# Optimization experiments

Measured on AMD Instinct MI355X. Metric: run time of the kernel, lower is better.

## Reference

```python
import jax, jax.numpy as jnp
import numpy as np

N = 100000   # nodes
E = 1600000  # edges
F = 128      # input features
H = 128      # hidden
O = 64       # output classes
BN_EPS = 1e-5


def gcn_conv(x, edge_index, W, b, n_nodes):
    """PyG-style GCNConv: h = D^-1/2 (A+I) D^-1/2 (x W) + b."""
    h = x @ W  # [N, out]
    row = jnp.concatenate([edge_index[0], jnp.arange(n_nodes)])  # add self loops
    col = jnp.concatenate([edge_index[1], jnp.arange(n_nodes)])
    deg = jax.ops.segment_sum(jnp.ones_like(row, dtype=h.dtype), row, num_segments=n_nodes)
    dinv = jnp.where(deg > 0, jax.lax.rsqrt(deg), 0.0)
    norm = dinv[row] * dinv[col]                 # [E+N]
    msg = h[col] * norm[:, None]                 # gather + scale
    out = jax.ops.segment_sum(msg, row, num_segments=n_nodes)  # scatter-add
    return out + b


def batch_norm(x, gamma, beta):
    mean = jnp.mean(x, axis=0)
    var = jnp.var(x, axis=0)
    return (x - mean) * jax.lax.rsqrt(var + BN_EPS) * gamma + beta


def setup_inputs() -> dict:
    key = jax.random.key(0)
    ks = jax.random.split(key, 10)
    x = jax.random.normal(ks[0], (N, F), dtype=jnp.float32)
    edge_index = jax.random.randint(ks[1], (2, E), 0, N, dtype=jnp.int64)
    W1 = jax.random.normal(ks[2], (F, H), dtype=jnp.float32) / np.sqrt(F)
    b1 = jnp.zeros((H,), dtype=jnp.float32)
    gamma1 = jnp.ones((H,), dtype=jnp.float32)
    beta1 = jnp.zeros((H,), dtype=jnp.float32)
    W2 = jax.random.normal(ks[3], (H, H), dtype=jnp.float32) / np.sqrt(H)
    b2 = jnp.zeros((H,), dtype=jnp.float32)
    W3 = jax.random.normal(ks[4], (H, O), dtype=jnp.float32) / np.sqrt(H)
    b3 = jnp.zeros((O,), dtype=jnp.float32)
    return {"x": x, "edge_index": edge_index, "W1": W1, "b1": b1,
            "gamma1": gamma1, "beta1": beta1, "W2": W2, "b2": b2,
            "W3": W3, "b3": b3}


def reference(x, edge_index, W1, b1, gamma1, beta1, W2, b2, W3, b3):
    h = gcn_conv(x, edge_index, W1, b1, N)
    h = jax.nn.relu(batch_norm(h, gamma1, beta1))
    h = gcn_conv(h, edge_index, W2, b2, N)
    h = jax.nn.relu(h)
    out = h @ W3 + b3  # final Linear classifier head [N, O]
    return out
```

## Files before the change

kernel.cpp:

```cpp
#include <hip/hip_runtime.h>

#define NN 100000
#define EE 1600000
#define HN 128
#define OO 64
#define SB 256
#define NBUCK 196
#define CH 4096
#define SLAB 16384

typedef __attribute__((ext_vector_type(8))) short bf16x8;
typedef __attribute__((ext_vector_type(4))) float f32x4;

__device__ __forceinline__ unsigned short f2bf(float f){
  unsigned u = __float_as_uint(f);
  return (unsigned short)((u + 0x7FFFu + ((u >> 16) & 1u)) >> 16);
}
__device__ __forceinline__ float bflo(unsigned u){ return __uint_as_float(u << 16); }
__device__ __forceinline__ float bfhi(unsigned u){ return __uint_as_float(u & 0xFFFF0000u); }

__global__ __launch_bounds__(256) void k_bucket(const int* __restrict__ rows, const int* __restrict__ cols,
                                                int* __restrict__ pcur, unsigned* __restrict__ ebuf,
                                                const float* __restrict__ W1, const float* __restrict__ W2,
                                                const float* __restrict__ W3,
                                                unsigned short* __restrict__ Wp1, unsigned short* __restrict__ Wp2,
                                                unsigned short* __restrict__ Wp3){
  __shared__ int bc[NBUCK];
  __shared__ int boff[NBUCK];
  __shared__ int ccur[NBUCK];
  __shared__ int gbase[NBUCK];
  __shared__ uint2 stage[CH];
  const int t = threadIdx.x;
  const int base = blockIdx.x * CH;
  const int nval = min(CH, EE - base);

  for (int i = t; i < NBUCK; i += 256) bc[i] = 0;
  __syncthreads();

  int er[16], ec[16];
  #pragma unroll
  for (int j = 0; j < 16; ++j){
    int i = j*256 + t;
    if (i < nval){
      er[j] = rows[base+i]; ec[j] = cols[base+i];
      atomicAdd(&bc[er[j] >> 9], 1);
    } else er[j] = -1;
  }
  __syncthreads();

  if (t < 64){
    int lane = t, run = 0;
    for (int c = 0; c < NBUCK; c += 64){
      int i = c + lane;
      int v = (i < NBUCK) ? bc[i] : 0;
      int s = v;
      #pragma unroll
      for (int d = 1; d < 64; d <<= 1){ int u = __shfl_up(s, d); if (lane >= d) s += u; }
      if (i < NBUCK) boff[i] = run + s - v;
      run += __shfl(s, 63);
    }
  }
  __syncthreads();
  if (t < NBUCK){
    gbase[t] = bc[t] ? (t*SLAB + atomicAdd(&pcur[t], bc[t])) : 0;
    ccur[t]  = boff[t];
  }
  __syncthreads();
  #pragma unroll
  for (int j = 0; j < 16; ++j){
    if (er[j] >= 0){
      int b = er[j] >> 9;
      int p = atomicAdd(&ccur[b], 1);
      stage[p] = make_uint2((unsigned)er[j], (unsigned)ec[j]);
    }
  }
  __syncthreads();
  for (int i = t; i < nval; i += 256){
    uint2 e = stage[i];
    int b = (int)(e.x >> 9);
    unsigned pk = ((e.x & 511u) << 17) | e.y;
    ebuf[gbase[b] + (i - boff[b])] = pk;
  }

  int b = blockIdx.x;
  if (b < 20){
    const float* W; unsigned short* Wp; int outc, i0;
    if (b < 8)      { W=W1; Wp=Wp1; outc=128; i0 = b*256; }
    else if (b < 16){ W=W2; Wp=Wp2; outc=128; i0 = (b-8)*256; }
    else            { W=W3; Wp=Wp3; outc=64;  i0 = (b-16)*256; }
    int i = i0 + t;
    if (i < 16*outc){
      int kb = i / outc, n = i - kb*outc;
      unsigned pk[4];
      #pragma unroll
      for (int jj = 0; jj < 4; ++jj){
        unsigned lo = f2bf(W[(size_t)(kb*8 + 2*jj)*outc + n]);
        unsigned hi = f2bf(W[(size_t)(kb*8 + 2*jj+1)*outc + n]);
        pk[jj] = lo | (hi << 16);
      }
      *reinterpret_cast<uint4*>(Wp + (size_t)i*8) = make_uint4(pk[0],pk[1],pk[2],pk[3]);
    }
  }
}

__global__ __launch_bounds__(256) void k_build(const unsigned* __restrict__ ebuf,
                                               const int* __restrict__ pcur,
                                               int* __restrict__ row_start, int* __restrict__ cnt,
                                               float* __restrict__ dinv, int* __restrict__ csr_col){
  __shared__ int hist[512];
  __shared__ int cur[512];
  __shared__ int sCbase;
  const int b = blockIdx.x;
  const int row0 = b << 9;
  const int nrow = min(512, NN - row0);
  const int ebase = b * SLAB;
  const int ne = pcur[b];
  const int t = threadIdx.x;

  if (t < 64){
    int acc = 0;
    for (int i = t; i < b; i += 64) acc += pcur[i];
    #pragma unroll
    for (int d = 32; d; d >>= 1) acc += __shfl_xor(acc, d);
    if (t == 0) sCbase = acc;
  }
  for (int i = t; i < nrow; i += 256) hist[i] = 0;
  __syncthreads();
  for (int i = t; i < ne; i += 256)
    atomicAdd(&hist[ebuf[ebase+i] >> 17], 1);
  __syncthreads();

  if (t < 64){
    int lane = t, run = 0;
    for (int c = 0; c < nrow; c += 64){
      int i = c + lane;
      int v = (i < nrow) ? hist[i] : 0;
      int s = v;
      #pragma unroll
      for (int d = 1; d < 64; d <<= 1){ int u = __shfl_up(s, d); if (lane >= d) s += u; }
      if (i < nrow) cur[i] = run + s - v;
      run += __shfl(s, 63);
    }
  }
  __syncthreads();
  const int cbase = sCbase;
  for (int i = t; i < nrow; i += 256){
    int h = hist[i];
    int r = row0 + i;
    cnt[r] = h;
    dinv[r] = rsqrtf((float)(h+1));
    row_start[r] = cbase + cur[i];
    cur[i] += cbase;
  }
  __syncthreads();
  for (int i = t; i < ne; i += 256){
    unsigned e = ebuf[ebase+i];
    int p = atomicAdd(&cur[e >> 17], 1);
    csr_col[p] = (int)(e & 0x1FFFFu);
  }
}

__global__ __launch_bounds__(256) void k_agg(const unsigned* __restrict__ h,
                                             const int* __restrict__ row_start,
                                             const int* __restrict__ cnt,
                                             const int* __restrict__ col,
                                             const float* __restrict__ dinv,
                                             const float* __restrict__ bias,
                                             unsigned* __restrict__ outv){
  int wib  = __builtin_amdgcn_readfirstlane((int)(threadIdx.x >> 6));
  int wid  = blockIdx.x*4 + wib;
  int lane = threadIdx.x & 63;
  if (wid >= NN) return;
  int s = row_start[wid];
  int e = s + cnt[wid];
  float dr = dinv[wid];
  const unsigned* hp = h + lane;
  float ax, ay;
  {
    unsigned u = hp[(size_t)wid*64];
    ax = bflo(u); ay = bfhi(u);
  }
  int p = s;
  for (; p+7 < e; p += 8){
    unsigned uu[8];
    #pragma unroll
    for (int j=0;j<8;++j) uu[j] = hp[(size_t)col[p+j]*64];
    #pragma unroll
    for (int j=0;j<8;++j){ ax += bflo(uu[j]); ay += bfhi(uu[j]); }
  }
  for (; p+3 < e; p += 4){
    unsigned uu[4];
    #pragma unroll
    for (int j=0;j<4;++j) uu[j] = hp[(size_t)col[p+j]*64];
    #pragma unroll
    for (int j=0;j<4;++j){ ax += bflo(uu[j]); ay += bfhi(uu[j]); }
  }
  for (; p < e; ++p){
    unsigned u = hp[(size_t)col[p]*64];
    ax += bflo(u); ay += bfhi(u);
  }
  float2 bb = *reinterpret_cast<const float2*>(bias + 2*lane);
  float ox = ax*dr + bb.x, oy = ay*dr + bb.y;
  outv[(size_t)wid*64 + lane] = (unsigned)f2bf(ox) | ((unsigned)f2bf(oy) << 16);
}

template<int OUTC, int XFORM, bool BF16OUT, bool ABF16>
__global__ __launch_bounds__(256) void k_mgemm(const void* __restrict__ Av,
                                               const unsigned short* __restrict__ Wp,
                                               const float* __restrict__ scale,
                                               const float* __restrict__ shiftv,
                                               const float* __restrict__ bias,
                                               const float* __restrict__ dinv,
                                               void* __restrict__ Cv){
  __shared__ char AsB[32768];
  const int t = threadIdx.x;
  const int row0 = blockIdx.x * 128;

  if constexpr (ABF16){
    const uint4* A = (const uint4*)Av;
    const int c8 = t & 15;
    const int k0 = c8*8;
    float sc[8], sh[8];
    if (XFORM == 1){
      #pragma unroll
      for (int j=0;j<8;++j){ sc[j]=scale[k0+j]; sh[j]=shiftv[k0+j]; }
    }
    #pragma unroll
    for (int g = 0; g < 8; ++g){
      int f = g*256 + t;
      int r = f >> 4;
      int row = row0 + r;
      int rc = row < NN ? row : NN-1;
      uint4 q = A[(size_t)rc*16 + c8];
      float vf[8] = { bflo(q.x),bfhi(q.x),bflo(q.y),bfhi(q.y),
                      bflo(q.z),bfhi(q.z),bflo(q.w),bfhi(q.w) };
      if (XFORM == 1){
        #pragma unroll
        for (int j=0;j<8;++j) vf[j] = fmaxf(fmaf(vf[j], sc[j], sh[j]), 0.f);
      } else if (XFORM == 2){
        #pragma unroll
        for (int j=0;j<8;++j) vf[j] = fmaxf(vf[j], 0.f);
      }
      unsigned pk[4];
      #pragma unroll
      for (int j=0;j<4;++j)
        pk[j] = (unsigned)f2bf(vf[2*j]) | ((unsigned)f2bf(vf[2*j+1]) << 16);
      int boff = (c8*16) ^ ((r & 7) << 4);
      *reinterpret_cast<uint4*>(AsB + r*256 + boff) = make_uint4(pk[0],pk[1],pk[2],pk[3]);
    }
  } else {
    const float* A = (const float*)Av;
    #pragma unroll
    for (int g = 0; g < 16; ++g){
      int f = g*256 + t;
      int r = f >> 5;
      int c4 = f & 31;
      int row = row0 + r;
      int rc = row < NN ? row : NN-1;
      float4 v = *reinterpret_cast<const float4*>(A + (size_t)rc*HN + c4*4);
      if (XFORM == 2){
        v.x = fmaxf(v.x, 0.f); v.y = fmaxf(v.y, 0.f);
        v.z = fmaxf(v.z, 0.f); v.w = fmaxf(v.w, 0.f);
      }
      unsigned p0 = (unsigned)f2bf(v.x) | ((unsigned)f2bf(v.y) << 16);
      unsigned p1 = (unsigned)f2bf(v.z) | ((unsigned)f2bf(v.w) << 16);
      int boff = (c4*8) ^ ((r & 7) << 4);
      *reinterpret_cast<uint2*>(AsB + r*256 + boff) = make_uint2(p0, p1);
    }
  }
  __syncthreads();

  const int wv = t >> 6;
  const int l  = t & 63;
  const int lm = l & 15;
  const int lk = l >> 4;
  constexpr int NF = OUTC/16;

  f32x4 acc[2][NF];
  #pragma unroll
  for (int mi=0;mi<2;++mi)
    #pragma unroll
    for (int ni=0;ni<NF;++ni) acc[mi][ni] = (f32x4){0.f,0.f,0.f,0.f};

  const bf16x8* WpV = reinterpret_cast<const bf16x8*>(Wp);

  #pragma unroll
  for (int ks = 0; ks < 4; ++ks){
    bf16x8 af[2];
    #pragma unroll
    for (int mi=0;mi<2;++mi){
      int R = wv*32 + mi*16 + lm;
      int boff = (ks*64 + lk*16) ^ ((R & 7) << 4);
      af[mi] = *reinterpret_cast<const bf16x8*>(AsB + R*256 + boff);
    }
    int kb = ks*4 + lk;
    #pragma unroll
    for (int ni=0;ni<NF;++ni){
      int n = ni*16 + lm;
      bf16x8 bfr = WpV[kb*OUTC + n];
      acc[0][ni] = __builtin_amdgcn_mfma_f32_16x16x32_bf16(af[0], bfr, acc[0][ni], 0,0,0);
      acc[1][ni] = __builtin_amdgcn_mfma_f32_16x16x32_bf16(af[1], bfr, acc[1][ni], 0,0,0);
    }
  }

  #pragma unroll
  for (int mi=0;mi<2;++mi){
    #pragma unroll
    for (int j=0;j<4;++j){
      int grow = row0 + wv*32 + mi*16 + lk*4 + j;
      if (grow >= NN) continue;
      if constexpr (BF16OUT){
        float dr = dinv[grow];
        unsigned short* po = (unsigned short*)Cv + (size_t)grow*OUTC;
        #pragma unroll
        for (int ni=0;ni<NF;++ni)
          po[ni*16 + lm] = f2bf(acc[mi][ni][j] * dr);
      } else {
        float* po = (float*)Cv + (size_t)grow*OUTC;
        #pragma unroll
        for (int ni=0;ni<NF;++ni)
          po[ni*16 + lm] = acc[mi][ni][j] + bias[ni*16 + lm];
      }
    }
  }
}

__global__ __launch_bounds__(256) void k_stats(const unsigned* __restrict__ a,
                                               float* __restrict__ ps, float* __restrict__ pq){
  __shared__ float l0[256], l1[256], m0[256], m1[256];
  int c = threadIdx.x & 63;
  int grp = threadIdx.x >> 6;
  float s0=0.f,s1=0.f,q0=0.f,q1=0.f;
  for (int r = blockIdx.x*4 + grp; r < NN; r += SB*4){
    unsigned u = a[(size_t)r*64 + c];
    float v0 = bflo(u), v1 = bfhi(u);
    s0 += v0; s1 += v1; q0 = fmaf(v0,v0,q0); q1 = fmaf(v1,v1,q1);
  }
  l0[threadIdx.x]=s0; l1[threadIdx.x]=s1; m0[threadIdx.x]=q0; m1[threadIdx.x]=q1;
  __syncthreads();
  if (grp==0){
    #pragma unroll
    for (int g=1;g<4;++g){ s0+=l0[g*64+c]; s1+=l1[g*64+c]; q0+=m0[g*64+c]; q1+=m1[g*64+c]; }
    ps[blockIdx.x*128 + 2*c]   = s0; ps[blockIdx.x*128 + 2*c+1] = s1;
    pq[blockIdx.x*128 + 2*c]   = q0; pq[blockIdx.x*128 + 2*c+1] = q1;
  }
}

__global__ __launch_bounds__(128) void k_bnfinal(const float* __restrict__ ps, const float* __restrict__ pq,
                                                 const float* __restrict__ gamma, const float* __restrict__ beta,
                                                 float* __restrict__ scale, float* __restrict__ shiftv){
  int c = threadIdx.x;
  float s=0.f, q=0.f;
  for (int b=0;b<SB;b++){ s += ps[b*128+c]; q += pq[b*128+c]; }
  float mean = s * (1.0f/NN);
  float var  = q * (1.0f/NN) - mean*mean;
  float inv  = rsqrtf(var + 1e-5f);
  float sc = gamma[c]*inv;
  scale[c]  = sc;
  shiftv[c] = beta[c] - mean*sc;
}

extern "C" void kernel_launch(void* const* d_in, const int* in_sizes, int n_in,
                              void* d_out, int out_size, void* d_ws, size_t ws_size,
                              hipStream_t stream) {
  const float* x      = (const float*)d_in[0];
  const int*   ei     = (const int*)d_in[1];
  const int*   rows   = ei;
  const int*   cols   = ei + EE;
  const float* W1     = (const float*)d_in[2];
  const float* b1     = (const float*)d_in[3];
  const float* gamma1 = (const float*)d_in[4];
  const float* beta1  = (const float*)d_in[5];
  const float* W2     = (const float*)d_in[6];
  const float* b2     = (const float*)d_in[7];
  const float* W3     = (const float*)d_in[8];
  const float* b3     = (const float*)d_in[9];
  float* out = (float*)d_out;

  char* w = (char*)d_ws;
  float* buf0      = (float*)w; w += (size_t)NN*HN*4;
  float* buf1      = (float*)w; w += (size_t)NN*HN*4;
  int*   csr_col   = (int*)w;   w += (size_t)EE*4;
  int*   row_start = (int*)w;   w += (size_t)NN*4;
  int*   cnt       = (int*)w;   w += (size_t)NN*4;
  float* dinv      = (float*)w; w += (size_t)NN*4;
  float* ps        = (float*)w; w += (size_t)SB*128*4;
  float* pq        = (float*)w; w += (size_t)SB*128*4;
  float* scale     = (float*)w; w += 1024;
  float* shiftv    = (float*)w; w += 1024;
  int*   scr0      = (int*)w;   w += 4096;
  unsigned short* Wp1 = (unsigned short*)w; w += 128*128*2;
  unsigned short* Wp2 = (unsigned short*)w; w += 128*128*2;
  unsigned short* Wp3 = (unsigned short*)w; w += 128*64*2;
  int* pcur = scr0;
  unsigned* ebuf = (unsigned*)buf0;
  unsigned* hbf  = (unsigned*)buf0;
  unsigned* abf  = (unsigned*)buf1;

  (void)hipMemsetAsync(scr0, 0, 4096, stream);

  const int CB = (EE + CH - 1)/CH, GB = (NN+127)/128, AB = NN/4;

  k_bucket<<<CB, 256, 0, stream>>>(rows, cols, pcur, ebuf, W1, W2, W3, Wp1, Wp2, Wp3);
  k_build <<<NBUCK, 256, 0, stream>>>(ebuf, pcur, row_start, cnt, dinv, csr_col);

  k_mgemm<128,0,true,false><<<GB, 256, 0, stream>>>(x, Wp1, nullptr, nullptr, nullptr, dinv, hbf);
  k_agg<<<AB, 256, 0, stream>>>(hbf, row_start, cnt, csr_col, dinv, b1, abf);
  k_stats<<<SB, 256, 0, stream>>>(abf, ps, pq);
  k_bnfinal<<<1, 128, 0, stream>>>(ps, pq, gamma1, beta1, scale, shiftv);

  k_mgemm<128,1,true,true><<<GB, 256, 0, stream>>>(abf, Wp2, scale, shiftv, nullptr, dinv, hbf);
  k_agg<<<AB, 256, 0, stream>>>(hbf, row_start, cnt, csr_col, dinv, b2, abf);

  k_mgemm<64,2,false,true><<<GB, 256, 0, stream>>>(abf, Wp3, nullptr, nullptr, b3, nullptr, out);
}
```

Baseline: 257.8 us.

## Fuse first GEMM into bucketing kernel and fuse second aggregation with classifier GEMM

The first dense GEMM (x·W1) now runs in the same launch as the edge-bucketing kernel using separate block ranges, with W1 packed to bf16 per block in LDS. This works because the GEMM no longer needs dinv, which is instead applied per neighbor inside the first aggregation. The second aggregation is fused with ReLU and the final 128→64 classifier GEMM via an LDS tile, which removes one intermediate write and read. In exchange, the first aggregation does an extra dinv gather per edge, each GEMM block repacks W1 redundantly, and the edge buffer moves to the second half of buf0.

```diff
diff --git a/kernel.cpp b/kernel.cpp
--- a/kernel.cpp
+++ b/kernel.cpp
@@ -19,86 +19,172 @@
 __device__ __forceinline__ float bflo(unsigned u){ return __uint_as_float(u << 16); }
 __device__ __forceinline__ float bfhi(unsigned u){ return __uint_as_float(u & 0xFFFF0000u); }
 
-__global__ __launch_bounds__(256) void k_bucket(const int* __restrict__ rows, const int* __restrict__ cols,
-                                                int* __restrict__ pcur, unsigned* __restrict__ ebuf,
-                                                const float* __restrict__ W1, const float* __restrict__ W2,
-                                                const float* __restrict__ W3,
-                                                unsigned short* __restrict__ Wp1, unsigned short* __restrict__ Wp2,
-                                                unsigned short* __restrict__ Wp3){
-  __shared__ int bc[NBUCK];
-  __shared__ int boff[NBUCK];
-  __shared__ int ccur[NBUCK];
-  __shared__ int gbase[NBUCK];
-  __shared__ uint2 stage[CH];
+#define CB ((EE + CH - 1)/CH)
+#define GB ((NN + 127)/128)
+
+__global__ __launch_bounds__(256) void k_fused(const int* __restrict__ rows, const int* __restrict__ cols,
+                                               int* __restrict__ pcur, unsigned* __restrict__ ebuf,
+                                               const float* __restrict__ x, const float* __restrict__ W1,
+                                               const float* __restrict__ W2, const float* __restrict__ W3,
+                                               unsigned short* __restrict__ Wp2, unsigned short* __restrict__ Wp3,
+                                               unsigned* __restrict__ hbf){
+  __shared__ char lds[65536];
   const int t = threadIdx.x;
-  const int base = blockIdx.x * CH;
-  const int nval = min(CH, EE - base);
-
-  for (int i = t; i < NBUCK; i += 256) bc[i] = 0;
-  __syncthreads();
-
-  int er[16], ec[16];
-  #pragma unroll
-  for (int j = 0; j < 16; ++j){
-    int i = j*256 + t;
-    if (i < nval){
-      er[j] = rows[base+i]; ec[j] = cols[base+i];
-      atomicAdd(&bc[er[j] >> 9], 1);
-    } else er[j] = -1;
-  }
-  __syncthreads();
-
-  if (t < 64){
-    int lane = t, run = 0;
-    for (int c = 0; c < NBUCK; c += 64){
-      int i = c + lane;
-      int v = (i < NBUCK) ? bc[i] : 0;
-      int s = v;
-      #pragma unroll
-      for (int d = 1; d < 64; d <<= 1){ int u = __shfl_up(s, d); if (lane >= d) s += u; }
-      if (i < NBUCK) boff[i] = run + s - v;
-      run += __shfl(s, 63);
-    }
-  }
-  __syncthreads();
-  if (t < NBUCK){
-    gbase[t] = bc[t] ? (t*SLAB + atomicAdd(&pcur[t], bc[t])) : 0;
-    ccur[t]  = boff[t];
-  }
-  __syncthreads();
-  #pragma unroll
-  for (int j = 0; j < 16; ++j){
-    if (er[j] >= 0){
-      int b = er[j] >> 9;
-      int p = atomicAdd(&ccur[b], 1);
-      stage[p] = make_uint2((unsigned)er[j], (unsigned)ec[j]);
-    }
-  }
-  __syncthreads();
-  for (int i = t; i < nval; i += 256){
-    uint2 e = stage[i];
-    int b = (int)(e.x >> 9);
-    unsigned pk = ((e.x & 511u) << 17) | e.y;
-    ebuf[gbase[b] + (i - boff[b])] = pk;
-  }
-
-  int b = blockIdx.x;
-  if (b < 20){
-    const float* W; unsigned short* Wp; int outc, i0;
-    if (b < 8)      { W=W1; Wp=Wp1; outc=128; i0 = b*256; }
-    else if (b < 16){ W=W2; Wp=Wp2; outc=128; i0 = (b-8)*256; }
-    else            { W=W3; Wp=Wp3; outc=64;  i0 = (b-16)*256; }
-    int i = i0 + t;
-    if (i < 16*outc){
-      int kb = i / outc, n = i - kb*outc;
-      unsigned pk[4];
-      #pragma unroll
-      for (int jj = 0; jj < 4; ++jj){
-        unsigned lo = f2bf(W[(size_t)(kb*8 + 2*jj)*outc + n]);
-        unsigned hi = f2bf(W[(size_t)(kb*8 + 2*jj+1)*outc + n]);
-        pk[jj] = lo | (hi << 16);
-      }
-      *reinterpret_cast<uint4*>(Wp + (size_t)i*8) = make_uint4(pk[0],pk[1],pk[2],pk[3]);
+
+  if (blockIdx.x < CB){
+    int* bc    = (int*)lds;
+    int* boff  = (int*)(lds + 1024);
+    int* ccur  = (int*)(lds + 2048);
+    int* gbase = (int*)(lds + 3072);
+    uint2* stage = (uint2*)(lds + 4096);
+    const int base = blockIdx.x * CH;
+    const int nval = min(CH, EE - base);
+
+    for (int i = t; i < NBUCK; i += 256) bc[i] = 0;
+    __syncthreads();
+
+    int er[16], ec[16];
+    #pragma unroll
+    for (int j = 0; j < 16; ++j){
+      int i = j*256 + t;
+      if (i < nval){
+        er[j] = rows[base+i]; ec[j] = cols[base+i];
+        atomicAdd(&bc[er[j] >> 9], 1);
+      } else er[j] = -1;
+    }
+    __syncthreads();
+
+    if (t < 64){
+      int lane = t, run = 0;
+      for (int c = 0; c < NBUCK; c += 64){
+        int i = c + lane;
+        int v = (i < NBUCK) ? bc[i] : 0;
+        int s = v;
+        #pragma unroll
+        for (int d = 1; d < 64; d <<= 1){ int u = __shfl_up(s, d); if (lane >= d) s += u; }
+        if (i < NBUCK) boff[i] = run + s - v;
+        run += __shfl(s, 63);
+      }
+    }
+    __syncthreads();
+    if (t < NBUCK){
+      gbase[t] = bc[t] ? (t*SLAB + atomicAdd(&pcur[t], bc[t])) : 0;
+      ccur[t]  = boff[t];
+    }
+    __syncthreads();
+    #pragma unroll
+    for (int j = 0; j < 16; ++j){
+      if (er[j] >= 0){
+        int b = er[j] >> 9;
+        int p = atomicAdd(&ccur[b], 1);
+        stage[p] = make_uint2((unsigned)er[j], (unsigned)ec[j]);
+      }
+    }
+    __syncthreads();
+    for (int i = t; i < nval; i += 256){
+      uint2 e = stage[i];
+      int b = (int)(e.x >> 9);
+      unsigned pk = ((e.x & 511u) << 17) | e.y;
+      ebuf[gbase[b] + (i - boff[b])] = pk;
+    }
+
+    int b = blockIdx.x;
+    if (b < 12){
+      const float* W = (b < 8) ? W2 : W3;
+      unsigned short* Wp = (b < 8) ? Wp2 : Wp3;
+      int outc = (b < 8) ? 128 : 64;
+      int i0 = (b < 8) ? b*256 : (b-8)*256;
+      int i = i0 + t;
+      if (i < 16*outc){
+        int kb = i / outc, n = i - kb*outc;
+        unsigned pk[4];
+        #pragma unroll
+        for (int jj = 0; jj < 4; ++jj){
+          unsigned lo = f2bf(W[(size_t)(kb*8 + 2*jj)*outc + n]);
+          unsigned hi = f2bf(W[(size_t)(kb*8 + 2*jj+1)*outc + n]);
+          pk[jj] = lo | (hi << 16);
+        }
+        *reinterpret_cast<uint4*>(Wp + (size_t)i*8) = make_uint4(pk[0],pk[1],pk[2],pk[3]);
+      }
+    }
+  } else {
+    char* AsB = lds;
+    char* WsB = lds + 32768;
+    const int row0 = (int)(blockIdx.x - CB) * 128;
+
+    {
+      #pragma unroll
+      for (int it = 0; it < 8; ++it){
+        int i = it*256 + t;
+        int kb = i >> 7, n = i & 127;
+        unsigned pk[4];
+        #pragma unroll
+        for (int j = 0; j < 4; ++j){
+          unsigned lo = f2bf(W1[(size_t)(kb*8 + 2*j)*128 + n]);
+          unsigned hi = f2bf(W1[(size_t)(kb*8 + 2*j+1)*128 + n]);
+          pk[j] = lo | (hi << 16);
+        }
+        *reinterpret_cast<uint4*>(WsB + (size_t)i*16) = make_uint4(pk[0],pk[1],pk[2],pk[3]);
+      }
+    }
+    {
+      #pragma unroll
+      for (int g = 0; g < 16; ++g){
+        int f = g*256 + t;
+        int r = f >> 5;
+        int c4 = f & 31;
+        int row = row0 + r;
+        int rc = row < NN ? row : NN-1;
+        float4 v = *reinterpret_cast<const float4*>(x + (size_t)rc*HN + c4*4);
+        unsigned p0 = (unsigned)f2bf(v.x) | ((unsigned)f2bf(v.y) << 16);
+        unsigned p1 = (unsigned)f2bf(v.z) | ((unsigned)f2bf(v.w) << 16);
+        int boffb = (c4*8) ^ ((r & 7) << 4);
+        *reinterpret_cast<uint2*>(AsB + r*256 + boffb) = make_uint2(p0, p1);
+      }
+    }
+    __syncthreads();
+
+    const int wv = t >> 6;
+    const int l  = t & 63;
+    const int lm = l & 15;
+    const int lk = l >> 4;
+
+    f32x4 acc[2][8];
+    #pragma unroll
+    for (int mi=0;mi<2;++mi)
+      #pragma unroll
+      for (int ni=0;ni<8;++ni) acc[mi][ni] = (f32x4){0.f,0.f,0.f,0.f};
+
+    #pragma unroll
+    for (int ks = 0; ks < 4; ++ks){
+      bf16x8 af[2];
+      #pragma unroll
+      for (int mi=0;mi<2;++mi){
+        int R = wv*32 + mi*16 + lm;
+        int boffb = (ks*64 + lk*16) ^ ((R & 7) << 4);
+        af[mi] = *reinterpret_cast<const bf16x8*>(AsB + R*256 + boffb);
+      }
+      int kb = ks*4 + lk;
+      #pragma unroll
+      for (int ni=0;ni<8;++ni){
+        int n = ni*16 + lm;
+        bf16x8 bfr = *reinterpret_cast<const bf16x8*>(WsB + (size_t)(kb*128 + n)*16);
+        acc[0][ni] = __builtin_amdgcn_mfma_f32_16x16x32_bf16(af[0], bfr, acc[0][ni], 0,0,0);
+        acc[1][ni] = __builtin_amdgcn_mfma_f32_16x16x32_bf16(af[1], bfr, acc[1][ni], 0,0,0);
+      }
+    }
+
+    #pragma unroll
+    for (int mi=0;mi<2;++mi){
+      #pragma unroll
+      for (int j=0;j<4;++j){
+        int grow = row0 + wv*32 + mi*16 + lk*4 + j;
+        if (grow >= NN) continue;
+        unsigned short* po = (unsigned short*)hbf + (size_t)grow*HN;
+        #pragma unroll
+        for (int ni=0;ni<8;++ni)
+          po[ni*16 + lm] = f2bf(acc[mi][ni][j]);
+      }
     }
   }
 }
@@ -160,13 +246,13 @@
   }
 }
 
-__global__ __launch_bounds__(256) void k_agg(const unsigned* __restrict__ h,
-                                             const int* __restrict__ row_start,
-                                             const int* __restrict__ cnt,
-                                             const int* __restrict__ col,
-                                             const float* __restrict__ dinv,
-                                             const float* __restrict__ bias,
-                                             unsigned* __restrict__ outv){
+__global__ __launch_bounds__(256) void k_aggd(const unsigned* __restrict__ h,
+                                              const int* __restrict__ row_start,
+                                              const int* __restrict__ cnt,
+                                              const int* __restrict__ col,
+                                              const float* __restrict__ dinv,
+                                              const float* __restrict__ bias,
+                                              unsigned* __restrict__ outv){
   int wib  = __builtin_amdgcn_readfirstlane((int)(threadIdx.x >> 6));
   int wid  = blockIdx.x*4 + wib;
   int lane = threadIdx.x & 63;
@@ -178,53 +264,133 @@
   float ax, ay;
   {
     unsigned u = hp[(size_t)wid*64];
-    ax = bflo(u); ay = bfhi(u);
+    ax = dr*bflo(u); ay = dr*bfhi(u);
   }
   int p = s;
   for (; p+7 < e; p += 8){
-    unsigned uu[8];
-    #pragma unroll
-    for (int j=0;j<8;++j) uu[j] = hp[(size_t)col[p+j]*64];
-    #pragma unroll
-    for (int j=0;j<8;++j){ ax += bflo(uu[j]); ay += bfhi(uu[j]); }
+    unsigned uu[8]; float dd[8];
+    #pragma unroll
+    for (int j=0;j<8;++j){ int c = col[p+j]; dd[j] = dinv[c]; uu[j] = hp[(size_t)c*64]; }
+    #pragma unroll
+    for (int j=0;j<8;++j){ ax = fmaf(bflo(uu[j]), dd[j], ax); ay = fmaf(bfhi(uu[j]), dd[j], ay); }
   }
   for (; p+3 < e; p += 4){
-    unsigned uu[4];
-    #pragma unroll
-    for (int j=0;j<4;++j) uu[j] = hp[(size_t)col[p+j]*64];
-    #pragma unroll
-    for (int j=0;j<4;++j){ ax += bflo(uu[j]); ay += bfhi(uu[j]); }
+    unsigned uu[4]; float dd[4];
+    #pragma unroll
+    for (int j=0;j<4;++j){ int c = col[p+j]; dd[j] = dinv[c]; uu[j] = hp[(size_t)c*64]; }
+    #pragma unroll
+    for (int j=0;j<4;++j){ ax = fmaf(bflo(uu[j]), dd[j], ax); ay = fmaf(bfhi(uu[j]), dd[j], ay); }
   }
   for (; p < e; ++p){
-    unsigned u = hp[(size_t)col[p]*64];
-    ax += bflo(u); ay += bfhi(u);
+    int c = col[p]; float d = dinv[c];
+    unsigned u = hp[(size_t)c*64];
+    ax = fmaf(bflo(u), d, ax); ay = fmaf(bfhi(u), d, ay);
   }
   float2 bb = *reinterpret_cast<const float2*>(bias + 2*lane);
   float ox = ax*dr + bb.x, oy = ay*dr + bb.y;
   outv[(size_t)wid*64 + lane] = (unsigned)f2bf(ox) | ((unsigned)f2bf(oy) << 16);
 }
 
-template<int OUTC, int XFORM, bool BF16OUT, bool ABF16>
-__global__ __launch_bounds__(256) void k_mgemm(const void* __restrict__ Av,
-                                               const unsigned short* __restrict__ Wp,
-                                               const float* __restrict__ scale,
-                                               const float* __restrict__ shiftv,
-                                               const float* __restrict__ bias,
+__global__ __launch_bounds__(256) void k_aggmm(const unsigned* __restrict__ h,
+                                               const int* __restrict__ row_start,
+                                               const int* __restrict__ cnt,
+                                               const int* __restrict__ col,
                                                const float* __restrict__ dinv,
-                                               void* __restrict__ Cv){
+                                               const float* __restrict__ b2,
+                                               const unsigned short* __restrict__ Wp3,
+                                               const float* __restrict__ b3,
+                                               float* __restrict__ out){
+  __shared__ char AsB[32*256];
+  const int t = threadIdx.x;
+  const int wv = __builtin_amdgcn_readfirstlane(t >> 6);
+  const int lane = t & 63;
+  const int tile = blockIdx.x * 32;
+
+  for (int k = 0; k < 8; ++k){
+    int wid = tile + wv*8 + k;
+    int s = row_start[wid];
+    int e = s + cnt[wid];
+    float dr = dinv[wid];
+    const unsigned* hp = h + lane;
+    float ax, ay;
+    { unsigned u = hp[(size_t)wid*64]; ax = bflo(u); ay = bfhi(u); }
+    int p = s;
+    for (; p+7 < e; p += 8){
+      unsigned uu[8];
+      #pragma unroll
+      for (int j=0;j<8;++j) uu[j] = hp[(size_t)col[p+j]*64];
+      #pragma unroll
+      for (int j=0;j<8;++j){ ax += bflo(uu[j]); ay += bfhi(uu[j]); }
+    }
+    for (; p+3 < e; p += 4){
+      unsigned uu[4];
+      #pragma unroll
+      for (int j=0;j<4;++j) uu[j] = hp[(size_t)col[p+j]*64];
+      #pragma unroll
+      for (int j=0;j<4;++j){ ax += bflo(uu[j]); ay += bfhi(uu[j]); }
+    }
+    for (; p < e; ++p){
+      unsigned u = hp[(size_t)col[p]*64];
+      ax += bflo(u); ay += bfhi(u);
+    }
+    float2 bb = *reinterpret_cast<const float2*>(b2 + 2*lane);
+    float ox = fmaxf(ax*dr + bb.x, 0.f);
+    float oy = fmaxf(ay*dr + bb.y, 0.f);
+    int r = wv*8 + k;
+    unsigned pk = (unsigned)f2bf(ox) | ((unsigned)f2bf(oy) << 16);
+    *reinterpret_cast<unsigned*>(AsB + r*256 + ((lane*4) ^ ((r & 7) << 4))) = pk;
+  }
+  __syncthreads();
+
+  const int lm = lane & 15;
+  const int lk = lane >> 4;
+  const int mb  = wv >> 1;
+  const int nb2 = (wv & 1) * 2;
+  f32x4 acc[2] = {(f32x4){0.f,0.f,0.f,0.f},(f32x4){0.f,0.f,0.f,0.f}};
+  const bf16x8* WpV = reinterpret_cast<const bf16x8*>(Wp3);
+
+  #pragma unroll
+  for (int ks = 0; ks < 4; ++ks){
+    int R = mb*16 + lm;
+    bf16x8 af = *reinterpret_cast<const bf16x8*>(AsB + R*256 + ((ks*64 + lk*16) ^ ((R & 7) << 4)));
+    int kb = ks*4 + lk;
+    #pragma unroll
+    for (int ni = 0; ni < 2; ++ni){
+      int n = (nb2+ni)*16 + lm;
+      bf16x8 bfr = WpV[kb*OO + n];
+      acc[ni] = __builtin_amdgcn_mfma_f32_16x16x32_bf16(af, bfr, acc[ni], 0,0,0);
+    }
+  }
+
+  #pragma unroll
+  for (int ni = 0; ni < 2; ++ni){
+    int gcol = (nb2+ni)*16 + lm;
+    float bb = b3[gcol];
+    #pragma unroll
+    for (int j = 0; j < 4; ++j){
+      int grow = tile + mb*16 + lk*4 + j;
+      out[(size_t)grow*OO + gcol] = acc[ni][j] + bb;
+    }
+  }
+}
+
+__global__ __launch_bounds__(256) void k_mgemm2(const unsigned* __restrict__ Av,
+                                                const unsigned short* __restrict__ Wp,
+                                                const float* __restrict__ scale,
+                                                const float* __restrict__ shiftv,
+                                                const float* __restrict__ dinv,
+                                                unsigned* __restrict__ Cv){
   __shared__ char AsB[32768];
   const int t = threadIdx.x;
   const int row0 = blockIdx.x * 128;
 
-  if constexpr (ABF16){
+  {
     const uint4* A = (const uint4*)Av;
     const int c8 = t & 15;
     const int k0 = c8*8;
     float sc[8], sh[8];
-    if (XFORM == 1){
-      #pragma unroll
-      for (int j=0;j<8;++j){ sc[j]=scale[k0+j]; sh[j]=shiftv[k0+j]; }
-    }
+    #pragma unroll
+    for (int j=0;j<8;++j){ sc[j]=scale[k0+j]; sh[j]=shiftv[k0+j]; }
     #pragma unroll
     for (int g = 0; g < 8; ++g){
       int f = g*256 + t;
@@ -234,38 +400,14 @@
       uint4 q = A[(size_t)rc*16 + c8];
       float vf[8] = { bflo(q.x),bfhi(q.x),bflo(q.y),bfhi(q.y),
                       bflo(q.z),bfhi(q.z),bflo(q.w),bfhi(q.w) };
-      if (XFORM == 1){
-        #pragma unroll
-        for (int j=0;j<8;++j) vf[j] = fmaxf(fmaf(vf[j], sc[j], sh[j]), 0.f);
-      } else if (XFORM == 2){
-        #pragma unroll
-        for (int j=0;j<8;++j) vf[j] = fmaxf(vf[j], 0.f);
-      }
+      #pragma unroll
+      for (int j=0;j<8;++j) vf[j] = fmaxf(fmaf(vf[j], sc[j], sh[j]), 0.f);
       unsigned pk[4];
       #pragma unroll
       for (int j=0;j<4;++j)
         pk[j] = (unsigned)f2bf(vf[2*j]) | ((unsigned)f2bf(vf[2*j+1]) << 16);
-      int boff = (c8*16) ^ ((r & 7) << 4);
-      *reinterpret_cast<uint4*>(AsB + r*256 + boff) = make_uint4(pk[0],pk[1],pk[2],pk[3]);
-    }
-  } else {
-    const float* A = (const float*)Av;
-    #pragma unroll
-    for (int g = 0; g < 16; ++g){
-      int f = g*256 + t;
-      int r = f >> 5;
-      int c4 = f & 31;
-      int row = row0 + r;
-      int rc = row < NN ? row : NN-1;
-      float4 v = *reinterpret_cast<const float4*>(A + (size_t)rc*HN + c4*4);
-      if (XFORM == 2){
-        v.x = fmaxf(v.x, 0.f); v.y = fmaxf(v.y, 0.f);
-        v.z = fmaxf(v.z, 0.f); v.w = fmaxf(v.w, 0.f);
-      }
-      unsigned p0 = (unsigned)f2bf(v.x) | ((unsigned)f2bf(v.y) << 16);
-      unsigned p1 = (unsigned)f2bf(v.z) | ((unsigned)f2bf(v.w) << 16);
-      int boff = (c4*8) ^ ((r & 7) << 4);
-      *reinterpret_cast<uint2*>(AsB + r*256 + boff) = make_uint2(p0, p1);
+      int boffb = (c8*16) ^ ((r & 7) << 4);
+      *reinterpret_cast<uint4*>(AsB + r*256 + boffb) = make_uint4(pk[0],pk[1],pk[2],pk[3]);
     }
   }
   __syncthreads();
@@ -274,13 +416,12 @@
   const int l  = t & 63;
   const int lm = l & 15;
   const int lk = l >> 4;
-  constexpr int NF = OUTC/16;
-
-  f32x4 acc[2][NF];
+
+  f32x4 acc[2][8];
   #pragma unroll
   for (int mi=0;mi<2;++mi)
     #pragma unroll
-    for (int ni=0;ni<NF;++ni) acc[mi][ni] = (f32x4){0.f,0.f,0.f,0.f};
+    for (int ni=0;ni<8;++ni) acc[mi][ni] = (f32x4){0.f,0.f,0.f,0.f};
 
   const bf16x8* WpV = reinterpret_cast<const bf16x8*>(Wp);
 
@@ -290,14 +431,14 @@
     #pragma unroll
     for (int mi=0;mi<2;++mi){
       int R = wv*32 + mi*16 + lm;
-      int boff = (ks*64 + lk*16) ^ ((R & 7) << 4);
-      af[mi] = *reinterpret_cast<const bf16x8*>(AsB + R*256 + boff);
+      int boffb = (ks*64 + lk*16) ^ ((R & 7) << 4);
+      af[mi] = *reinterpret_cast<const bf16x8*>(AsB + R*256 + boffb);
     }
     int kb = ks*4 + lk;
     #pragma unroll
-    for (int ni=0;ni<NF;++ni){
+    for (int ni=0;ni<8;++ni){
       int n = ni*16 + lm;
-      bf16x8 bfr = WpV[kb*OUTC + n];
+      bf16x8 bfr = WpV[kb*128 + n];
       acc[0][ni] = __builtin_amdgcn_mfma_f32_16x16x32_bf16(af[0], bfr, acc[0][ni], 0,0,0);
       acc[1][ni] = __builtin_amdgcn_mfma_f32_16x16x32_bf16(af[1], bfr, acc[1][ni], 0,0,0);
     }
@@ -309,18 +450,11 @@
     for (int j=0;j<4;++j){
       int grow = row0 + wv*32 + mi*16 + lk*4 + j;
       if (grow >= NN) continue;
-      if constexpr (BF16OUT){
-        float dr = dinv[grow];
-        unsigned short* po = (unsigned short*)Cv + (size_t)grow*OUTC;
-        #pragma unroll
-        for (int ni=0;ni<NF;++ni)
-          po[ni*16 + lm] = f2bf(acc[mi][ni][j] * dr);
-      } else {
-        float* po = (float*)Cv + (size_t)grow*OUTC;
-        #pragma unroll
-        for (int ni=0;ni<NF;++ni)
-          po[ni*16 + lm] = acc[mi][ni][j] + bias[ni*16 + lm];
-      }
+      float dr = dinv[grow];
+      unsigned short* po = (unsigned short*)Cv + (size_t)grow*HN;
+      #pragma unroll
+      for (int ni=0;ni<8;++ni)
+        po[ni*16 + lm] = f2bf(acc[mi][ni][j] * dr);
     }
   }
 }
@@ -389,28 +523,25 @@
   float* scale     = (float*)w; w += 1024;
   float* shiftv    = (float*)w; w += 1024;
   int*   scr0      = (int*)w;   w += 4096;
-  unsigned short* Wp1 = (unsigned short*)w; w += 128*128*2;
   unsigned short* Wp2 = (unsigned short*)w; w += 128*128*2;
   unsigned short* Wp3 = (unsigned short*)w; w += 128*64*2;
   int* pcur = scr0;
-  unsigned* ebuf = (unsigned*)buf0;
   unsigned* hbf  = (unsigned*)buf0;
+  unsigned* ebuf = (unsigned*)buf0 + (size_t)NN*64;
   unsigned* abf  = (unsigned*)buf1;
 
   (void)hipMemsetAsync(scr0, 0, 4096, stream);
 
-  const int CB = (EE + CH - 1)/CH, GB = (NN+127)/128, AB = NN/4;
-
-  k_bucket<<<CB, 256, 0, stream>>>(rows, cols, pcur, ebuf, W1, W2, W3, Wp1, Wp2, Wp3);
-  k_build <<<NBUCK, 256, 0, stream>>>(ebuf, pcur, row_start, cnt, dinv, csr_col);
-
-  k_mgemm<128,0,true,false><<<GB, 256, 0, stream>>>(x, Wp1, nullptr, nullptr, nullptr, dinv, hbf);
-  k_agg<<<AB, 256, 0, stream>>>(hbf, row_start, cnt, csr_col, dinv, b1, abf);
+  const int AB = NN/4, FB = NN/32;
+
+  k_fused<<<CB + GB, 256, 0, stream>>>(rows, cols, pcur, ebuf, x, W1, W2, W3, Wp2, Wp3, hbf);
+  k_build<<<NBUCK, 256, 0, stream>>>(ebuf, pcur, row_start, cnt, dinv, csr_col);
+
+  k_aggd<<<AB, 256, 0, stream>>>(hbf, row_start, cnt, csr_col, dinv, b1, abf);
   k_stats<<<SB, 256, 0, stream>>>(abf, ps, pq);
   k_bnfinal<<<1, 128, 0, stream>>>(ps, pq, gamma1, beta1, scale, shiftv);
 
-  k_mgemm<128,1,true,true><<<GB, 256, 0, stream>>>(abf, Wp2, scale, shiftv, nullptr, dinv, hbf);
-  k_agg<<<AB, 256, 0, stream>>>(hbf, row_start, cnt, csr_col, dinv, b2, abf);
-
-  k_mgemm<64,2,false,true><<<GB, 256, 0, stream>>>(abf, Wp3, nullptr, nullptr, b3, nullptr, out);
-}
+  k_mgemm2<<<GB, 256, 0, stream>>>(abf, Wp2, scale, shiftv, dinv, hbf);
+
+  k_aggmm<<<FB, 256, 0, stream>>>(hbf, row_start, cnt, csr_col, dinv, b2, Wp3, b3, out);
+}
```

Result: faster. 240.0 us, median of 2 (-6.9%).
